# Performance work log

Measured on AMD Instinct MI355X. Metric: run time of the kernel, lower is better.

## Reference

```python
import jax, jax.numpy as jnp
import numpy as np
from jax import lax

NUM_GROUPS = 16
GN_EPS = 1e-5
POOL = 4
CLAMP_MIN, CLAMP_MAX = 0.0, 1.0


def setup_inputs() -> dict:
    key = jax.random.key(0)
    ks = jax.random.split(key, 4)
    x = jax.random.normal(ks[0], (128, 8, 128, 128), dtype=jnp.float32)
    conv_weight = jax.random.normal(ks[1], (64, 8, 3, 3), dtype=jnp.float32) * 0.1
    conv_bias = jax.random.normal(ks[2], (64,), dtype=jnp.float32) * 0.1
    gn_weight = jnp.ones((64,), dtype=jnp.float32)
    gn_bias = jnp.zeros((64,), dtype=jnp.float32)
    scale = jax.random.normal(ks[3], (64, 1, 1), dtype=jnp.float32)
    return {"x": x, "conv_weight": conv_weight, "conv_bias": conv_bias,
            "gn_weight": gn_weight, "gn_bias": gn_bias, "scale": scale}


def reference(x, conv_weight, conv_bias, gn_weight, gn_bias, scale):
    # Conv2d (stride=1, padding=0)
    y = lax.conv_general_dilated(
        x, conv_weight, window_strides=(1, 1), padding='VALID',
        dimension_numbers=('NCHW', 'OIHW', 'NCHW'))
    y = y + conv_bias[None, :, None, None]  # [B, C, H, W] = [128, 64, 126, 126]

    # GroupNorm over (channels-in-group, H, W) per sample
    B, C, H, W = y.shape
    yg = y.reshape(B, NUM_GROUPS, C // NUM_GROUPS, H, W)
    mean = jnp.mean(yg, axis=(2, 3, 4), keepdims=True)
    var = jnp.var(yg, axis=(2, 3, 4), keepdims=True)
    yn = ((yg - mean) * lax.rsqrt(var + GN_EPS)).reshape(B, C, H, W)
    yn = yn * gn_weight[None, :, None, None] + gn_bias[None, :, None, None]

    # scale (broadcast [C,1,1])
    yn = yn * scale[None]

    # MaxPool2d(kernel=4, stride=4)
    p = lax.reduce_window(yn, -jnp.inf, lax.max,
                          window_dimensions=(1, 1, POOL, POOL),
                          window_strides=(1, 1, POOL, POOL),
                          padding='VALID')  # [128, 64, 31, 31]

    # clamp
    return jnp.clip(p, CLAMP_MIN, CLAMP_MAX)
```

## Files before the change

### kernel.cpp

```cpp
#include <hip/hip_runtime.h>
#include <math.h>

typedef _Float16 f16x8 __attribute__((ext_vector_type(8)));
typedef float f32x4 __attribute__((ext_vector_type(4)));

#define CIN 8
#define HIN 128
#define WIN 128
#define OH 126
#define OW 126
#define COUT 64
#define NB 128
#define NGROUPS 16
#define CPG 4
#define PWN 31
#define XROWS 35

#define NPOOL (NB*PWN*PWN*COUT)
#define OFF_PART (NPOOL/2)
#define NPART (NB*NGROUPS*16*2)

__global__ __launch_bounds__(256, 4)
void conv_mfma_kernel(const float* __restrict__ x,
                      const float* __restrict__ w,
                      const float* __restrict__ bias,
                      const float* __restrict__ gnw,
                      const float* __restrict__ scale,
                      float* __restrict__ ws)
{
  __shared__ __align__(16) _Float16 xs[XROWS*34*8];
  __shared__ __align__(16) _Float16 wls[12*64*8];
  __shared__ float red[4][16][2];

  const int tid  = threadIdx.x;
  const int lane = tid & 63, wave = tid >> 6;
  const int tileIdx = blockIdx.x;
  const int tx = tileIdx & 3, ty = tileIdx >> 2;
  const int b  = blockIdx.y;
  const int ox0 = tx*32, oy0 = ty*32;

  for (int idx = tid; idx < 12*64*8; idx += 256) {
    const int ci = idx & 7, n = (idx >> 3) & 63, khw = idx >> 9;
    const float v = (khw < 9) ? w[(n*CIN + ci)*9 + khw] : 0.f;
    wls[idx] = (_Float16)v;
  }

  const float* xb = x + (size_t)b * CIN*HIN*WIN;
  for (int p = tid; p < XROWS*34; p += 256) {
    const int r = p / 34, c = p - r*34;
    const int iy = oy0 + r, ix = ox0 + c;
    const bool ok = (iy < HIN) && (ix < WIN);
    const int gbase = iy*WIN + ix;
    f16x8 pk;
    #pragma unroll
    for (int ci = 0; ci < 8; ++ci) {
      const float v = ok ? xb[ci*HIN*WIN + gbase] : 0.f;
      pk[ci] = (_Float16)v;
    }
    *(f16x8*)&xs[p*8] = pk;
  }
  __syncthreads();

  const int q = lane >> 4, ln = lane & 15;

  f16x8 bf[4][3];
  #pragma unroll
  for (int nt = 0; nt < 4; ++nt)
    #pragma unroll
    for (int c = 0; c < 3; ++c)
      bf[nt][c] = *(const f16x8*)&wls[((c*4 + q)*64 + nt*16 + ln)*8];

  const int dy = ln >> 2, dx = ln & 3;
  int aoff[3];
  #pragma unroll
  for (int c = 0; c < 3; ++c) {
    const int khw = c*4 + q;
    const int ky = khw / 3, kx = khw - 3*(khw/3);
    aoff[c] = ((dy + ky)*34 + (dx + kx))*8;
  }

  float bias_r[4], sgn[4];
  #pragma unroll
  for (int nt = 0; nt < 4; ++nt) {
    const int c = nt*16 + ln;
    bias_r[nt] = bias[c];
    sgn[nt] = (gnw[c]*scale[c] >= 0.f) ? 1.f : -1.f;
  }

  float s[4]  = {0.f,0.f,0.f,0.f};
  float sq[4] = {0.f,0.f,0.f,0.f};
  _Float16* wext = (_Float16*)ws;

  #pragma unroll 2
  for (int i = 0; i < 16; ++i) {
    const int wyl = wave*2 + (i >> 3), wxl = i & 7;
    const int base = (wyl*4*34 + wxl*4)*8;

    f32x4 acc[4];
    #pragma unroll
    for (int nt = 0; nt < 4; ++nt) {
      const float bv = bias_r[nt];
      acc[nt] = (f32x4){bv, bv, bv, bv};
    }
    #pragma unroll
    for (int c = 0; c < 3; ++c) {
      const f16x8 a = *(const f16x8*)&xs[base + aoff[c]];
      #pragma unroll
      for (int nt = 0; nt < 4; ++nt)
        acc[nt] = __builtin_amdgcn_mfma_f32_16x16x32_f16(a, bf[nt][c], acc[nt], 0, 0, 0);
    }

    const int wyg = ty*8 + wyl, wxg = tx*8 + wxl;
    if ((wyg < PWN) && (wxg < PWN)) {
      const size_t rowbase = ((size_t)(b*PWN + wyg)*PWN + wxg)*COUT;
      #pragma unroll
      for (int nt = 0; nt < 4; ++nt) {
        const float v0 = acc[nt][0], v1 = acc[nt][1];
        const float v2 = acc[nt][2], v3 = acc[nt][3];
        s[nt]  += (v0+v1) + (v2+v3);
        sq[nt] += v0*v0 + v1*v1 + v2*v2 + v3*v3;
        const float sg = sgn[nt];
        float m = fmaxf(fmaxf(sg*v0, sg*v1), fmaxf(sg*v2, sg*v3));
        m = fmaxf(m, __shfl_xor(m, 16, 64));
        m = fmaxf(m, __shfl_xor(m, 32, 64));
        if (lane < 16) wext[rowbase + nt*16 + ln] = (_Float16)(sg*m);
      }
    } else {
      const bool yv = (wyg*4 + q) < OH;
      #pragma unroll
      for (int nt = 0; nt < 4; ++nt) {
        #pragma unroll
        for (int r = 0; r < 4; ++r) {
          const bool okp = yv && (wxg*4 + r < OW);
          const float v = okp ? acc[nt][r] : 0.f;
          s[nt] += v; sq[nt] += v*v;
        }
      }
    }
  }

  #pragma unroll
  for (int nt = 0; nt < 4; ++nt) {
    float a = s[nt], c2 = sq[nt];
    a  += __shfl_xor(a, 16, 64);  a  += __shfl_xor(a, 32, 64);
    a  += __shfl_xor(a, 1, 64);   a  += __shfl_xor(a, 2, 64);
    c2 += __shfl_xor(c2, 16, 64); c2 += __shfl_xor(c2, 32, 64);
    c2 += __shfl_xor(c2, 1, 64);  c2 += __shfl_xor(c2, 2, 64);
    if (lane < 16 && (lane & 3) == 0) {
      red[wave][nt*4 + (ln >> 2)][0] = a;
      red[wave][nt*4 + (ln >> 2)][1] = c2;
    }
  }
  __syncthreads();
  if (tid < 32) {
    const int g = tid >> 1, k = tid & 1;
    const float t = red[0][g][k] + red[1][g][k] + red[2][g][k] + red[3][g][k];
    ws[OFF_PART + (((size_t)b*NGROUPS + g)*16 + tileIdx)*2 + k] = t;
  }
}

__global__ __launch_bounds__(256)
void finalize_kernel(const float* __restrict__ gnw,
                     const float* __restrict__ gnb,
                     const float* __restrict__ scale,
                     const float* __restrict__ ws,
                     float* __restrict__ out)
{
  __shared__ float stat[NGROUPS][2];
  __shared__ float As[COUT], Bs[COUT];
  __shared__ float vout[COUT*PWN];

  const int tid = threadIdx.x;
  const int wy  = blockIdx.x;
  const int b   = blockIdx.y;

  if (tid < NGROUPS) {
    const float* p = ws + OFF_PART + ((size_t)(b*NGROUPS + tid))*32;
    float s = 0.f, sq = 0.f;
    #pragma unroll
    for (int t = 0; t < 16; ++t) { s += p[t*2]; sq += p[t*2+1]; }
    const float N = (float)(CPG * OH * OW);
    const float mean = s / N;
    const float var  = sq / N - mean*mean;
    stat[tid][0] = mean;
    stat[tid][1] = rsqrtf(var + 1e-5f);
  }
  __syncthreads();
  if (tid < COUT) {
    const int c = tid, g = c >> 2;
    const float ag = stat[g][1] * gnw[c];
    As[c] = ag * scale[c];
    Bs[c] = (gnb[c] - stat[g][0] * ag) * scale[c];
  }
  __syncthreads();

  const _Float16* wext = (const _Float16*)ws;
  const size_t rb = (size_t)(b*PWN + wy)*PWN*COUT;
  for (int idx = tid; idx < PWN*COUT; idx += 256) {
    const int c = idx & 63, wx = idx >> 6;
    const float ext = (float)wext[rb + idx];
    float v = fmaf(As[c], ext, Bs[c]);
    v = fminf(fmaxf(v, 0.f), 1.f);
    vout[c*PWN + wx] = v;
  }
  __syncthreads();

  for (int idx = tid; idx < COUT*PWN; idx += 256) {
    const int c = idx / PWN, wx = idx - c*PWN;
    out[(((size_t)b*COUT + c)*PWN + wy)*PWN + wx] = vout[idx];
  }
}

extern "C" void kernel_launch(void* const* d_in, const int* in_sizes, int n_in,
                              void* d_out, int out_size, void* d_ws, size_t ws_size,
                              hipStream_t stream)
{
  const float* x     = (const float*)d_in[0];
  const float* cw    = (const float*)d_in[1];
  const float* cb    = (const float*)d_in[2];
  const float* gnw   = (const float*)d_in[3];
  const float* gnb   = (const float*)d_in[4];
  const float* scale = (const float*)d_in[5];
  float* out = (float*)d_out;
  float* ws  = (float*)d_ws;

  dim3 gridA(16, NB, 1);
  conv_mfma_kernel<<<gridA, 256, 0, stream>>>(x, cw, cb, gnw, scale, ws);

  dim3 gridF(PWN, NB, 1);
  finalize_kernel<<<gridF, 256, 0, stream>>>(gnw, gnb, scale, ws, out);
}
```

Measured before the change: 194.3 us.

## Fuse GroupNorm finalize into conv kernel via last-block atomic counter

Removes the separate finalize kernel. Each batch sample counts its finished tile blocks with an atomic counter, and the last of its 16 blocks reduces the group statistics and writes all 31 pooled rows for that sample. The pooled-max store is also rewritten so all 64 lanes write one value each instead of four masked 16-lane stores. In exchange, the finalize work for a sample now runs serially in one block, which creates a tail. A small kernel is added to zero the counters each call.

```diff
diff --git a/kernel.cpp b/kernel.cpp
--- a/kernel.cpp
+++ b/kernel.cpp
@@ -19,18 +19,27 @@
 #define NPOOL (NB*PWN*PWN*COUT)
 #define OFF_PART (NPOOL/2)
 #define NPART (NB*NGROUPS*16*2)
+#define OFF_CNT (OFF_PART + NPART)
+
+__global__ void zero_cnt_kernel(float* __restrict__ ws)
+{
+  ((int*)(ws + OFF_CNT))[threadIdx.x] = 0;
+}
 
 __global__ __launch_bounds__(256, 4)
 void conv_mfma_kernel(const float* __restrict__ x,
                       const float* __restrict__ w,
                       const float* __restrict__ bias,
                       const float* __restrict__ gnw,
+                      const float* __restrict__ gnb,
                       const float* __restrict__ scale,
-                      float* __restrict__ ws)
+                      float* __restrict__ ws,
+                      float* __restrict__ out)
 {
   __shared__ __align__(16) _Float16 xs[XROWS*34*8];
   __shared__ __align__(16) _Float16 wls[12*64*8];
   __shared__ float red[4][16][2];
+  __shared__ int winner;
 
   const int tid  = threadIdx.x;
   const int lane = tid & 63, wave = tid >> 6;
@@ -113,6 +122,7 @@
     const int wyg = ty*8 + wyl, wxg = tx*8 + wxl;
     if ((wyg < PWN) && (wxg < PWN)) {
       const size_t rowbase = ((size_t)(b*PWN + wyg)*PWN + wxg)*COUT;
+      float m4[4];
       #pragma unroll
       for (int nt = 0; nt < 4; ++nt) {
         const float v0 = acc[nt][0], v1 = acc[nt][1];
@@ -123,8 +133,13 @@
         float m = fmaxf(fmaxf(sg*v0, sg*v1), fmaxf(sg*v2, sg*v3));
         m = fmaxf(m, __shfl_xor(m, 16, 64));
         m = fmaxf(m, __shfl_xor(m, 32, 64));
-        if (lane < 16) wext[rowbase + nt*16 + ln] = (_Float16)(sg*m);
+        m4[nt] = sg*m;
       }
+      float mv = m4[0];
+      mv = (q == 1) ? m4[1] : mv;
+      mv = (q == 2) ? m4[2] : mv;
+      mv = (q == 3) ? m4[3] : mv;
+      wext[rowbase + lane] = (_Float16)mv;
     } else {
       const bool yv = (wyg*4 + q) < OH;
       #pragma unroll
@@ -157,57 +172,56 @@
     const float t = red[0][g][k] + red[1][g][k] + red[2][g][k] + red[3][g][k];
     ws[OFF_PART + (((size_t)b*NGROUPS + g)*16 + tileIdx)*2 + k] = t;
   }
-}
-
-__global__ __launch_bounds__(256)
-void finalize_kernel(const float* __restrict__ gnw,
-                     const float* __restrict__ gnb,
-                     const float* __restrict__ scale,
-                     const float* __restrict__ ws,
-                     float* __restrict__ out)
-{
-  __shared__ float stat[NGROUPS][2];
-  __shared__ float As[COUT], Bs[COUT];
-  __shared__ float vout[COUT*PWN];
-
-  const int tid = threadIdx.x;
-  const int wy  = blockIdx.x;
-  const int b   = blockIdx.y;
-
-  if (tid < NGROUPS) {
-    const float* p = ws + OFF_PART + ((size_t)(b*NGROUPS + tid))*32;
-    float s = 0.f, sq = 0.f;
-    #pragma unroll
-    for (int t = 0; t < 16; ++t) { s += p[t*2]; sq += p[t*2+1]; }
-    const float N = (float)(CPG * OH * OW);
-    const float mean = s / N;
-    const float var  = sq / N - mean*mean;
-    stat[tid][0] = mean;
-    stat[tid][1] = rsqrtf(var + 1e-5f);
+
+  __threadfence();
+  __syncthreads();
+  if (tid == 0)
+    winner = (atomicAdd((int*)(ws + OFF_CNT) + b, 1) == 15) ? 1 : 0;
+  __syncthreads();
+  if (!winner) return;
+  __threadfence();
+
+  float* fbuf = (float*)xs;
+  float* As   = fbuf;
+  float* Bs   = fbuf + 64;
+  float* vout = fbuf + 128;
+  float* stat_raw = (float*)red;
+
+  if (tid < 32) {
+    const float* p = ws + OFF_PART + (size_t)(b*NGROUPS + (tid >> 1))*32 + (tid & 1);
+    float acc0 = 0.f;
+    #pragma unroll
+    for (int t = 0; t < 16; ++t) acc0 += p[t*2];
+    stat_raw[tid] = acc0;
   }
   __syncthreads();
   if (tid < COUT) {
     const int c = tid, g = c >> 2;
-    const float ag = stat[g][1] * gnw[c];
+    const float N = (float)(CPG * OH * OW);
+    const float mean = stat_raw[g*2] / N;
+    const float var  = stat_raw[g*2 + 1] / N - mean*mean;
+    const float inv  = rsqrtf(var + 1e-5f);
+    const float ag   = inv * gnw[c];
     As[c] = ag * scale[c];
-    Bs[c] = (gnb[c] - stat[g][0] * ag) * scale[c];
-  }
-  __syncthreads();
-
-  const _Float16* wext = (const _Float16*)ws;
-  const size_t rb = (size_t)(b*PWN + wy)*PWN*COUT;
-  for (int idx = tid; idx < PWN*COUT; idx += 256) {
-    const int c = idx & 63, wx = idx >> 6;
-    const float ext = (float)wext[rb + idx];
-    float v = fmaf(As[c], ext, Bs[c]);
-    v = fminf(fmaxf(v, 0.f), 1.f);
-    vout[c*PWN + wx] = v;
-  }
-  __syncthreads();
-
-  for (int idx = tid; idx < COUT*PWN; idx += 256) {
-    const int c = idx / PWN, wx = idx - c*PWN;
-    out[(((size_t)b*COUT + c)*PWN + wy)*PWN + wx] = vout[idx];
+    Bs[c] = (gnb[c] - mean * ag) * scale[c];
+  }
+  __syncthreads();
+
+  const _Float16* wextr = (const _Float16*)ws;
+  for (int wy = 0; wy < PWN; ++wy) {
+    const size_t rb = (size_t)(b*PWN + wy)*PWN*COUT;
+    for (int idx = tid; idx < PWN*COUT; idx += 256) {
+      const int c = idx & 63, wx = idx >> 6;
+      float v = fmaf(As[c], (float)wextr[rb + idx], Bs[c]);
+      v = fminf(fmaxf(v, 0.f), 1.f);
+      vout[c*PWN + wx] = v;
+    }
+    __syncthreads();
+    for (int idx = tid; idx < COUT*PWN; idx += 256) {
+      const int c = idx / PWN, wx = idx - c*PWN;
+      out[(((size_t)b*COUT + c)*PWN + wy)*PWN + wx] = vout[idx];
+    }
+    __syncthreads();
   }
 }
 
@@ -224,9 +238,8 @@
   float* out = (float*)d_out;
   float* ws  = (float*)d_ws;
 
+  zero_cnt_kernel<<<1, NB, 0, stream>>>(ws);
+
   dim3 gridA(16, NB, 1);
-  conv_mfma_kernel<<<gridA, 256, 0, stream>>>(x, cw, cb, gnw, scale, ws);
-
-  dim3 gridF(PWN, NB, 1);
-  finalize_kernel<<<gridF, 256, 0, stream>>>(gnw, gnb, scale, ws, out);
+  conv_mfma_kernel<<<gridA, 256, 0, stream>>>(x, cw, cb, gnw, gnb, scale, ws, out);
 }
```

Result: slower. 603.0 us (+210.4%).

## Split finalize into per-batch affine prep and vectorized apply kernel, trim conv LDS

Applied to the files above, without the earlier changes.

The GroupNorm affine coefficients are now computed once per sample in a small prep kernel, instead of being recomputed by each of the 31 row blocks. A new apply kernel handles four pooled rows per block and reads the fp16 maxima with 16-byte vector loads. In the conv kernel, the x tile drops one padded row and the weight LDS drops the zero-padded taps; the unused MFMA lanes are zeroed in registers with their offsets clamped. The pooled max store is now one coalesced 64-lane write instead of four 16-lane writes. The cost is an extra kernel launch, plus apply blocks that loop with a sync per row.

```diff
diff --git a/kernel.cpp b/kernel.cpp
--- a/kernel.cpp
+++ b/kernel.cpp
@@ -14,11 +14,12 @@
 #define NGROUPS 16
 #define CPG 4
 #define PWN 31
-#define XROWS 35
+#define XROWS 34
 
 #define NPOOL (NB*PWN*PWN*COUT)
 #define OFF_PART (NPOOL/2)
 #define NPART (NB*NGROUPS*16*2)
+#define OFF_AB (OFF_PART + NPART)
 
 __global__ __launch_bounds__(256, 4)
 void conv_mfma_kernel(const float* __restrict__ x,
@@ -29,7 +30,7 @@
                       float* __restrict__ ws)
 {
   __shared__ __align__(16) _Float16 xs[XROWS*34*8];
-  __shared__ __align__(16) _Float16 wls[12*64*8];
+  __shared__ __align__(16) _Float16 wls[9*64*8];
   __shared__ float red[4][16][2];
 
   const int tid  = threadIdx.x;
@@ -39,10 +40,9 @@
   const int b  = blockIdx.y;
   const int ox0 = tx*32, oy0 = ty*32;
 
-  for (int idx = tid; idx < 12*64*8; idx += 256) {
+  for (int idx = tid; idx < 9*64*8; idx += 256) {
     const int ci = idx & 7, n = (idx >> 3) & 63, khw = idx >> 9;
-    const float v = (khw < 9) ? w[(n*CIN + ci)*9 + khw] : 0.f;
-    wls[idx] = (_Float16)v;
+    wls[idx] = (_Float16)w[(n*CIN + ci)*9 + khw];
   }
 
   const float* xb = x + (size_t)b * CIN*HIN*WIN;
@@ -65,10 +65,15 @@
 
   f16x8 bf[4][3];
   #pragma unroll
-  for (int nt = 0; nt < 4; ++nt)
-    #pragma unroll
-    for (int c = 0; c < 3; ++c)
+  for (int nt = 0; nt < 4; ++nt) {
+    #pragma unroll
+    for (int c = 0; c < 2; ++c)
       bf[nt][c] = *(const f16x8*)&wls[((c*4 + q)*64 + nt*16 + ln)*8];
+    if (q == 0)
+      bf[nt][2] = *(const f16x8*)&wls[((8)*64 + nt*16 + ln)*8];
+    else
+      bf[nt][2] = (f16x8){0,0,0,0,0,0,0,0};
+  }
 
   const int dy = ln >> 2, dx = ln & 3;
   int aoff[3];
@@ -76,7 +81,7 @@
   for (int c = 0; c < 3; ++c) {
     const int khw = c*4 + q;
     const int ky = khw / 3, kx = khw - 3*(khw/3);
-    aoff[c] = ((dy + ky)*34 + (dx + kx))*8;
+    aoff[c] = (khw < 9) ? ((dy + ky)*34 + (dx + kx))*8 : 0;
   }
 
   float bias_r[4], sgn[4];
@@ -113,6 +118,7 @@
     const int wyg = ty*8 + wyl, wxg = tx*8 + wxl;
     if ((wyg < PWN) && (wxg < PWN)) {
       const size_t rowbase = ((size_t)(b*PWN + wyg)*PWN + wxg)*COUT;
+      float m4[4];
       #pragma unroll
       for (int nt = 0; nt < 4; ++nt) {
         const float v0 = acc[nt][0], v1 = acc[nt][1];
@@ -123,8 +129,13 @@
         float m = fmaxf(fmaxf(sg*v0, sg*v1), fmaxf(sg*v2, sg*v3));
         m = fmaxf(m, __shfl_xor(m, 16, 64));
         m = fmaxf(m, __shfl_xor(m, 32, 64));
-        if (lane < 16) wext[rowbase + nt*16 + ln] = (_Float16)(sg*m);
+        m4[nt] = sg*m;
       }
+      float mv = m4[0];
+      mv = (q == 1) ? m4[1] : mv;
+      mv = (q == 2) ? m4[2] : mv;
+      mv = (q == 3) ? m4[3] : mv;
+      wext[rowbase + lane] = (_Float16)mv;
     } else {
       const bool yv = (wyg*4 + q) < OH;
       #pragma unroll
@@ -159,55 +170,69 @@
   }
 }
 
+__global__ __launch_bounds__(64)
+void prep_ab_kernel(const float* __restrict__ gnw,
+                    const float* __restrict__ gnb,
+                    const float* __restrict__ scale,
+                    float* __restrict__ ws)
+{
+  __shared__ float stat[NGROUPS*2];
+  const int tid = threadIdx.x, b = blockIdx.x;
+  if (tid < 32) {
+    const int g = tid >> 1, k = tid & 1;
+    const float* p = ws + OFF_PART + (size_t)(b*NGROUPS + g)*32 + k;
+    float a = 0.f;
+    #pragma unroll
+    for (int t = 0; t < 16; ++t) a += p[t*2];
+    stat[g*2 + k] = a;
+  }
+  __syncthreads();
+  const int c = tid, g = c >> 2;
+  const float N = (float)(CPG * OH * OW);
+  const float mean = stat[g*2] / N;
+  const float var  = stat[g*2 + 1] / N - mean*mean;
+  const float inv  = rsqrtf(var + 1e-5f);
+  const float ag   = inv * gnw[c];
+  ws[OFF_AB + b*128 + c]      = ag * scale[c];
+  ws[OFF_AB + b*128 + 64 + c] = (gnb[c] - mean * ag) * scale[c];
+}
+
 __global__ __launch_bounds__(256)
-void finalize_kernel(const float* __restrict__ gnw,
-                     const float* __restrict__ gnb,
-                     const float* __restrict__ scale,
-                     const float* __restrict__ ws,
-                     float* __restrict__ out)
-{
-  __shared__ float stat[NGROUPS][2];
-  __shared__ float As[COUT], Bs[COUT];
+void apply_kernel(const float* __restrict__ ws, float* __restrict__ out)
+{
+  __shared__ float AB[128];
   __shared__ float vout[COUT*PWN];
 
   const int tid = threadIdx.x;
-  const int wy  = blockIdx.x;
+  const int yq  = blockIdx.x;
   const int b   = blockIdx.y;
 
-  if (tid < NGROUPS) {
-    const float* p = ws + OFF_PART + ((size_t)(b*NGROUPS + tid))*32;
-    float s = 0.f, sq = 0.f;
-    #pragma unroll
-    for (int t = 0; t < 16; ++t) { s += p[t*2]; sq += p[t*2+1]; }
-    const float N = (float)(CPG * OH * OW);
-    const float mean = s / N;
-    const float var  = sq / N - mean*mean;
-    stat[tid][0] = mean;
-    stat[tid][1] = rsqrtf(var + 1e-5f);
-  }
-  __syncthreads();
-  if (tid < COUT) {
-    const int c = tid, g = c >> 2;
-    const float ag = stat[g][1] * gnw[c];
-    As[c] = ag * scale[c];
-    Bs[c] = (gnb[c] - stat[g][0] * ag) * scale[c];
-  }
+  if (tid < 128) AB[tid] = ws[OFF_AB + b*128 + tid];
   __syncthreads();
 
   const _Float16* wext = (const _Float16*)ws;
-  const size_t rb = (size_t)(b*PWN + wy)*PWN*COUT;
-  for (int idx = tid; idx < PWN*COUT; idx += 256) {
-    const int c = idx & 63, wx = idx >> 6;
-    const float ext = (float)wext[rb + idx];
-    float v = fmaf(As[c], ext, Bs[c]);
-    v = fminf(fmaxf(v, 0.f), 1.f);
-    vout[c*PWN + wx] = v;
-  }
-  __syncthreads();
-
-  for (int idx = tid; idx < COUT*PWN; idx += 256) {
-    const int c = idx / PWN, wx = idx - c*PWN;
-    out[(((size_t)b*COUT + c)*PWN + wy)*PWN + wx] = vout[idx];
+  for (int r = 0; r < 4; ++r) {
+    const int wy = yq*4 + r;
+    if (wy >= PWN) break;
+    const size_t rb = (size_t)(b*PWN + wy)*PWN*COUT;
+
+    if (tid < 248) {
+      const f16x8 e = *(const f16x8*)&wext[rb + tid*8];
+      const int wx = tid >> 3, c0 = (tid & 7)*8;
+      #pragma unroll
+      for (int j = 0; j < 8; ++j) {
+        const int c = c0 + j;
+        float v = fmaf(AB[c], (float)e[j], AB[64 + c]);
+        v = fminf(fmaxf(v, 0.f), 1.f);
+        vout[c*PWN + wx] = v;
+      }
+    }
+    __syncthreads();
+    for (int e = tid; e < COUT*PWN; e += 256) {
+      const int c = e / PWN, wx = e - c*PWN;
+      out[(((size_t)b*COUT + c)*PWN + wy)*PWN + wx] = vout[e];
+    }
+    __syncthreads();
   }
 }
 
@@ -227,6 +252,8 @@
   dim3 gridA(16, NB, 1);
   conv_mfma_kernel<<<gridA, 256, 0, stream>>>(x, cw, cb, gnw, scale, ws);
 
-  dim3 gridF(PWN, NB, 1);
-  finalize_kernel<<<gridF, 256, 0, stream>>>(gnw, gnb, scale, ws, out);
-}
+  prep_ab_kernel<<<NB, 64, 0, stream>>>(gnw, gnb, scale, ws);
+
+  dim3 gridP(8, NB, 1);
+  apply_kernel<<<gridP, 256, 0, stream>>>(ws, out);
+}
```

Result: faster. 185.1 us (-4.7%).
